# Kernel tuning notes

Measured on AMD Instinct MI355X. Metric: run time of the kernel, lower is better.

The kernel has to match this reference:

```python
import jax, jax.numpy as jnp
import numpy as np

VOCAB = 50257
INPUT_DIM = 1024
CUTOFF_ENDS = [0, 10000, 30000, VOCAB]
PROJ_DIMS = [1024, 512, 256]  # input_dim // factor**i, factor=2.0
N_TOKENS = 8192


def setup_inputs() -> dict:
    key = jax.random.key(0)
    ks = jax.random.split(key, 16)
    inp = {
        "x": jax.random.normal(ks[0], (N_TOKENS, INPUT_DIM), dtype=jnp.float32),
        "target": jax.random.randint(ks[1], (N_TOKENS,), 0, VOCAB, dtype=jnp.int64),
    }
    # Per-cluster projection weights (nn.Linear(input_dim, proj_dim, bias=False) -> [proj_dim, input_dim])
    # and output layers (nn.Linear(proj_dim, cluster_size) -> weight [cluster, proj_dim], bias [cluster]).
    for i in range(3):
        cluster = CUTOFF_ENDS[i + 1] - CUTOFF_ENDS[i]
        pd = PROJ_DIMS[i]
        inp[f"p{i}"] = jax.random.normal(ks[2 + 3 * i], (pd, INPUT_DIM), dtype=jnp.float32) * 0.02
        inp[f"w{i}"] = jax.random.normal(ks[3 + 3 * i], (cluster, pd), dtype=jnp.float32) * 0.02
        inp[f"b{i}"] = jnp.zeros((cluster,), dtype=jnp.float32)
    return inp


def reference(x, target, p0, w0, b0, p1, w1, b1, p2, w2, b2):
    # Faithful to torch AdaptiveSoftmax.forward(input, target):
    # per-cluster: gather tokens whose target falls in [l, r), project, classify,
    # cross-entropy. Clusters partition [0, vocab), so every token hits exactly
    # one cluster; we compute each cluster's pipeline densely over all tokens
    # (jit-friendly, no data-dependent shapes) and select per-token via the mask.
    projs, ws, bs = [p0, p1, p2], [w0, w1, w2], [b0, b1, b2]
    target = target.astype(jnp.int32)
    nll = jnp.zeros((x.shape[0],), dtype=x.dtype)
    for i in range(3):
        l, r = CUTOFF_ENDS[i], CUTOFF_ENDS[i + 1]
        mask = (target >= l) & (target < r)
        hidden = jnp.einsum('nd,pd->np', x, projs[i])          # [N, proj_dim]
        logits = jnp.einsum('np,cp->nc', hidden, ws[i]) + bs[i]  # [N, cluster]
        logp = jax.nn.log_softmax(logits, axis=-1)
        t_i = jnp.clip(target - l, 0, r - l - 1)
        nll_i = -jnp.take_along_axis(logp, t_i[:, None], axis=1)[:, 0]
        nll = jnp.where(mask, nll_i, nll)
    loss = nll.sum()  # == sum of per-cluster reduction='sum' cross-entropies
    return loss, nll
```

## Files before the change

kernel.cpp:

```cpp
#include <hip/hip_runtime.h>
#include <cmath>

#define N_TOK 8192
#define DIM 1024

using bf16x8 = __attribute__((ext_vector_type(8))) short;
using f32x4  = __attribute__((ext_vector_type(4))) float;

__device__ __forceinline__ unsigned f2bf(float f) {
  unsigned u = __float_as_uint(f);
  return (u + 0x7fffu + ((u >> 16) & 1u)) >> 16;
}

__device__ __forceinline__ void gll16(const void* g, void* l) {
  __builtin_amdgcn_global_load_lds(
      (const __attribute__((address_space(1))) void*)g,
      (__attribute__((address_space(3))) void*)l, 16, 0, 0);
}

__global__ __launch_bounds__(1024) void k_setup(const int* __restrict__ tgt,
                                                int* __restrict__ cnt,
                                                int* __restrict__ hoff,
                                                int* __restrict__ perm) {
  __shared__ int base[3];
  int t = threadIdx.x;
  if (t < 3) base[t] = 0;
  __syncthreads();
  for (int i = t; i < N_TOK; i += 1024) {
    int tg = tgt[i];
    int cid = (tg < 10000) ? 0 : (tg < 30000 ? 1 : 2);
    int slot = atomicAdd(&base[cid], 1);
    perm[cid * N_TOK + slot] = i;
  }
  __syncthreads();
  if (t < 3) cnt[t] = base[t];
  if (t == 0) {
    hoff[0] = 0;
    hoff[1] = base[0] * 1024;
    hoff[2] = base[0] * 1024 + base[1] * 512;
  }
}

__global__ __launch_bounds__(256) void k_hc(
    const float* __restrict__ x,
    const float* __restrict__ p0, const float* __restrict__ p1, const float* __restrict__ p2,
    const float* __restrict__ w0, const float* __restrict__ w1, const float* __restrict__ w2,
    const int* __restrict__ perm, const int* __restrict__ cnt, const int* __restrict__ hoffs,
    unsigned short* __restrict__ wb, unsigned short* __restrict__ hb) {
  if (blockIdx.z == 0) {
    const int nw0 = 10240000, nw1 = 10240000, nw2 = 5185792;
    const int total4 = (nw0 + nw1 + nw2) >> 2;
    for (int i = blockIdx.x * 256 + threadIdx.x; i < total4; i += 512 * 256) {
      int e = i << 2;
      const float* src;
      if (e < nw0) src = w0 + e;
      else if (e < nw0 + nw1) src = w1 + (e - nw0);
      else src = w2 + (e - nw0 - nw1);
      float4 v = *(const float4*)src;
      uint2 o;
      o.x = f2bf(v.x) | (f2bf(v.y) << 16);
      o.y = f2bf(v.z) | (f2bf(v.w) << 16);
      *(uint2*)(wb + e) = o;
    }
    return;
  }
  const int cid = blockIdx.z - 1;
  const int pd = (cid == 0) ? 1024 : (cid == 1) ? 512 : 256;
  const int count = cnt[cid];
  if (count == 0) return;
  const int nchd = pd >> 7;
  const int chunk = blockIdx.x % nchd;
  const int tile = blockIdx.x / nchd;
  if (tile * 128 >= count) return;
  const int dim0 = chunk * 128, row0 = tile * 128;
  const float* P = (cid == 0) ? p0 : (cid == 1) ? p1 : p2;
  const size_t hoff = (size_t)hoffs[cid];

  __shared__ char pool[34816];
  __shared__ int ptoks[128];
  short* stg = (short*)pool;
  short* Os = (short*)pool;

  const int t = threadIdx.x, wv = t >> 6, lane = t & 63, m = lane & 15, q = lane >> 4;
  const int wr = wv >> 1, wc = wv & 1;

  if (t < 128) {
    int idx = row0 + t;
    ptoks[t] = perm[cid * N_TOK + min(idx, count - 1)];
  }
  __syncthreads();

  const int s0 = t, s1 = t + 256;
  const int r0 = s0 >> 2, g0 = (s0 & 3) ^ ((r0 >> 1) & 3);
  const int r1 = s1 >> 2, g1 = (s1 & 3) ^ ((r1 >> 1) & 3);
  const uint4* srcA0 = (const uint4*)(x + (size_t)ptoks[r0] * DIM) + g0 * 2;
  const uint4* srcA1 = (const uint4*)(x + (size_t)ptoks[r1] * DIM) + g1 * 2;
  const uint4* srcB0 = (const uint4*)(P + (size_t)(dim0 + r0) * DIM) + g0 * 2;
  const uint4* srcB1 = (const uint4*)(P + (size_t)(dim0 + r1) * DIM) + g1 * 2;

  f32x4 acc[4][4];
  #pragma unroll
  for (int rt = 0; rt < 4; ++rt)
    #pragma unroll
    for (int ct = 0; ct < 4; ++ct) acc[rt][ct] = (f32x4){0.f, 0.f, 0.f, 0.f};

  const int sR = (q ^ ((m >> 1) & 3)) * 8;

  {
    uint4 a0 = srcA0[0], a1 = srcA0[1], a2 = srcA1[0], a3 = srcA1[1];
    uint4 b0 = srcB0[0], b1 = srcB0[1], b2 = srcB1[0], b3 = srcB1[1];
    uint4 o;
    o.x = (a0.x >> 16) | (a0.y & 0xFFFF0000u); o.y = (a0.z >> 16) | (a0.w & 0xFFFF0000u);
    o.z = (a1.x >> 16) | (a1.y & 0xFFFF0000u); o.w = (a1.z >> 16) | (a1.w & 0xFFFF0000u);
    *(uint4*)&stg[s0 * 8] = o;
    o.x = (a2.x >> 16) | (a2.y & 0xFFFF0000u); o.y = (a2.z >> 16) | (a2.w & 0xFFFF0000u);
    o.z = (a3.x >> 16) | (a3.y & 0xFFFF0000u); o.w = (a3.z >> 16) | (a3.w & 0xFFFF0000u);
    *(uint4*)&stg[s1 * 8] = o;
    o.x = (b0.x >> 16) | (b0.y & 0xFFFF0000u); o.y = (b0.z >> 16) | (b0.w & 0xFFFF0000u);
    o.z = (b1.x >> 16) | (b1.y & 0xFFFF0000u); o.w = (b1.z >> 16) | (b1.w & 0xFFFF0000u);
    *(uint4*)&stg[4096 + s0 * 8] = o;
    o.x = (b2.x >> 16) | (b2.y & 0xFFFF0000u); o.y = (b2.z >> 16) | (b2.w & 0xFFFF0000u);
    o.z = (b3.x >> 16) | (b3.y & 0xFFFF0000u); o.w = (b3.z >> 16) | (b3.w & 0xFFFF0000u);
    *(uint4*)&stg[4096 + s1 * 8] = o;
  }

  int p = 0;
  for (int ks = 0; ks < 32; ++ks) {
    __syncthreads();
    const bool nxt = (ks + 1) < 32;
    uint4 a0, a1, a2, a3, b0, b1, b2, b3;
    if (nxt) {
      int ko = (ks + 1) * 8;
      a0 = srcA0[ko]; a1 = srcA0[ko + 1]; a2 = srcA1[ko]; a3 = srcA1[ko + 1];
      b0 = srcB0[ko]; b1 = srcB0[ko + 1]; b2 = srcB1[ko]; b3 = srcB1[ko + 1];
    }
    short* SAp = stg + p * 8192;
    short* SBp = SAp + 4096;
    bf16x8 af[4];
    #pragma unroll
    for (int rt = 0; rt < 4; ++rt)
      af[rt] = *(bf16x8*)&SAp[(wr * 64 + rt * 16 + m) * 32 + sR];
    #pragma unroll
    for (int ct = 0; ct < 4; ++ct) {
      bf16x8 bb = *(bf16x8*)&SBp[(wc * 64 + ct * 16 + m) * 32 + sR];
      #pragma unroll
      for (int rt = 0; rt < 4; ++rt)
        acc[rt][ct] = __builtin_amdgcn_mfma_f32_16x16x32_bf16(af[rt], bb, acc[rt][ct], 0, 0, 0);
    }
    if (nxt) {
      short* DA = stg + (p ^ 1) * 8192;
      short* DB = DA + 4096;
      uint4 o;
      o.x = (a0.x >> 16) | (a0.y & 0xFFFF0000u); o.y = (a0.z >> 16) | (a0.w & 0xFFFF0000u);
      o.z = (a1.x >> 16) | (a1.y & 0xFFFF0000u); o.w = (a1.z >> 16) | (a1.w & 0xFFFF0000u);
      *(uint4*)&DA[s0 * 8] = o;
      o.x = (a2.x >> 16) | (a2.y & 0xFFFF0000u); o.y = (a2.z >> 16) | (a2.w & 0xFFFF0000u);
      o.z = (a3.x >> 16) | (a3.y & 0xFFFF0000u); o.w = (a3.z >> 16) | (a3.w & 0xFFFF0000u);
      *(uint4*)&DA[s1 * 8] = o;
      o.x = (b0.x >> 16) | (b0.y & 0xFFFF0000u); o.y = (b0.z >> 16) | (b0.w & 0xFFFF0000u);
      o.z = (b1.x >> 16) | (b1.y & 0xFFFF0000u); o.w = (b1.z >> 16) | (b1.w & 0xFFFF0000u);
      *(uint4*)&DB[s0 * 8] = o;
      o.x = (b2.x >> 16) | (b2.y & 0xFFFF0000u); o.y = (b2.z >> 16) | (b2.w & 0xFFFF0000u);
      o.z = (b3.x >> 16) | (b3.y & 0xFFFF0000u); o.w = (b3.z >> 16) | (b3.w & 0xFFFF0000u);
      *(uint4*)&DB[s1 * 8] = o;
    }
    p ^= 1;
  }

  __syncthreads();
  #pragma unroll
  for (int rt = 0; rt < 4; ++rt)
    #pragma unroll
    for (int ct = 0; ct < 4; ++ct)
      #pragma unroll
      for (int rr = 0; rr < 4; ++rr)
        Os[(wr * 64 + rt * 16 + q * 4 + rr) * 136 + wc * 64 + ct * 16 + m] =
            (short)f2bf(acc[rt][ct][rr]);
  __syncthreads();
  {
    int orow = t >> 1, oh = t & 1;
    int slot = row0 + orow;
    if (slot < count) {
      unsigned short* dst = hb + hoff + (size_t)slot * pd + dim0 + oh * 64;
      const short* src = &Os[orow * 136 + oh * 64];
      #pragma unroll
      for (int i = 0; i < 8; ++i)
        *(uint4*)(dst + i * 8) = *(const uint4*)(src + i * 8);
    }
  }
}

__global__ __launch_bounds__(256) void k_lse(
    const unsigned short* __restrict__ hb, const unsigned short* __restrict__ wb,
    const float* __restrict__ b0_, const float* __restrict__ b1_, const float* __restrict__ b2_,
    const int* __restrict__ tgt, const int* __restrict__ perm,
    const int* __restrict__ cnt, const int* __restrict__ hoffs,
    float* __restrict__ psum, float* __restrict__ tlog) {
  const int cid = blockIdx.z;
  const int pd     = (cid == 0) ? 1024  : (cid == 1) ? 512   : 256;
  const int cstart = (cid == 0) ? 0     : (cid == 1) ? 10000 : 30000;
  const int csize  = (cid == 0) ? 10000 : (cid == 1) ? 20000 : 20257;
  const size_t woff = (cid == 0) ? 0 : (cid == 1) ? (size_t)10240000 : (size_t)20480000;
  const float* bias = (cid == 0) ? b0_ : (cid == 1) ? b1_ : b2_;
  const int count = cnt[cid];
  if (count == 0) return;
  const unsigned ntile = (unsigned)(count + 127) >> 7;
  const int nchunk = (csize + 127) >> 7;
  const int cpx = (nchunk + 7) >> 3;

  const unsigned d = blockIdx.x;
  const int x8 = d & 7;
  const unsigned g = d >> 3;
  const unsigned ci = g / ntile;
  if (ci >= (unsigned)cpx) return;
  const int chunk = x8 * cpx + (int)ci;
  if (chunk >= nchunk) return;
  const int tile = (int)(g - ci * ntile);
  const int col0 = chunk * 128, row0 = tile * 128;
  const size_t hoff = (size_t)hoffs[cid];

  __shared__ short SA[2][4096];
  __shared__ short SB[2][4096];
  __shared__ int ptoks[128];
  __shared__ int tlocs[128];

  const int t = threadIdx.x, wv = t >> 6, lane = t & 63, m = lane & 15, q = lane >> 4;
  const int wr = wv >> 1, wc = wv & 1;

  if (t < 128) {
    int idx = row0 + t;
    int tok = perm[cid * N_TOK + min(idx, count - 1)];
    ptoks[t] = tok;
    tlocs[t] = tgt[tok] - cstart;
  }

  const int sub = lane >> 2;
  const int gsw = (lane & 3) ^ ((sub >> 1) & 3);
  const unsigned short *pA[2], *pB[2];
  short *lA[2][2], *lB[2][2];
  #pragma unroll
  for (int i = 0; i < 2; ++i) {
    int ia = wv * 2 + i;
    int ra = ia * 16 + sub;
    pA[i] = hb + hoff + (size_t)min(row0 + ra, count - 1) * pd + gsw * 8;
    pB[i] = wb + woff + (size_t)min(col0 + ra, csize - 1) * pd + gsw * 8;
    #pragma unroll
    for (int pp = 0; pp < 2; ++pp) {
      lA[i][pp] = &SA[pp][ia * 512];
      lB[i][pp] = &SB[pp][ia * 512];
    }
  }

  float bc[4];
  #pragma unroll
  for (int ct = 0; ct < 4; ++ct)
    bc[ct] = bias[min(col0 + wc * 64 + ct * 16 + m, csize - 1)];

  f32x4 acc[4][4];
  #pragma unroll
  for (int rt = 0; rt < 4; ++rt)
    #pragma unroll
    for (int ct = 0; ct < 4; ++ct) acc[rt][ct] = (f32x4){0.f, 0.f, 0.f, 0.f};

  const int sR = (q ^ ((m >> 1) & 3)) * 8;
  const int nk = pd >> 5;

  #pragma unroll
  for (int i = 0; i < 2; ++i) { gll16(pA[i], lA[i][0]); gll16(pB[i], lB[i][0]); }

  int p = 0;
  for (int ks = 0; ks < nk; ++ks) {
    __syncthreads();
    if (ks + 1 < nk) {
      int ko = (ks + 1) * 32;
      #pragma unroll
      for (int i = 0; i < 2; ++i) {
        gll16(pA[i] + ko, lA[i][p ^ 1]);
        gll16(pB[i] + ko, lB[i][p ^ 1]);
      }
    }
    bf16x8 af[4];
    #pragma unroll
    for (int rt = 0; rt < 4; ++rt)
      af[rt] = *(bf16x8*)&SA[p][(wr * 64 + rt * 16 + m) * 32 + sR];
    #pragma unroll
    for (int ct = 0; ct < 4; ++ct) {
      bf16x8 bb = *(bf16x8*)&SB[p][(wc * 64 + ct * 16 + m) * 32 + sR];
      #pragma unroll
      for (int rt = 0; rt < 4; ++rt)
        acc[rt][ct] = __builtin_amdgcn_mfma_f32_16x16x32_bf16(af[rt], bb, acc[rt][ct], 0, 0, 0);
    }
    p ^= 1;
  }

  float run[4][4] = {{0.f}}, tcap[4][4] = {{0.f}};
  int tfnd[4][4] = {{0}};
  int tl[4][4];
  #pragma unroll
  for (int rt = 0; rt < 4; ++rt)
    #pragma unroll
    for (int rr = 0; rr < 4; ++rr)
      tl[rt][rr] = tlocs[wr * 64 + rt * 16 + q * 4 + rr];

  #pragma unroll
  for (int ct = 0; ct < 4; ++ct) {
    int colg = col0 + wc * 64 + ct * 16 + m;
    bool cok = colg < csize;
    #pragma unroll
    for (int rt = 0; rt < 4; ++rt)
      #pragma unroll
      for (int rr = 0; rr < 4; ++rr) {
        float val = acc[rt][ct][rr] + bc[ct];
        if (cok) {
          run[rt][rr] += __expf(val);
          if (tl[rt][rr] == colg) { tcap[rt][rr] = val; tfnd[rt][rr] = 1; }
        }
      }
  }

  #pragma unroll
  for (int rt = 0; rt < 4; ++rt)
    #pragma unroll
    for (int rr = 0; rr < 4; ++rr) {
      float v = run[rt][rr];
      v += __shfl_xor(v, 1, 64);
      v += __shfl_xor(v, 2, 64);
      v += __shfl_xor(v, 4, 64);
      v += __shfl_xor(v, 8, 64);
      int rowl = wr * 64 + rt * 16 + q * 4 + rr;
      if (row0 + rowl < count) {
        int tok = ptoks[rowl];
        if (m == 0) atomicAdd(&psum[tok], v);
        if (tfnd[rt][rr]) tlog[tok] = tcap[rt][rr];
      }
    }
}

__global__ __launch_bounds__(1024) void k_final(const float* __restrict__ psum,
                                                const float* __restrict__ tlog,
                                                float* __restrict__ out) {
  __shared__ float part[16];
  int t = threadIdx.x;
  float s = 0.f;
  for (int n = t; n < N_TOK; n += 1024) {
    float v = __logf(psum[n]) - tlog[n];
    out[1 + n] = v;
    s += v;
  }
  #pragma unroll
  for (int off = 32; off > 0; off >>= 1) s += __shfl_down(s, off, 64);
  if ((t & 63) == 0) part[t >> 6] = s;
  __syncthreads();
  if (t < 64) {
    float v = (t < 16) ? part[t] : 0.f;
    #pragma unroll
    for (int off = 8; off > 0; off >>= 1) v += __shfl_down(v, off, 64);
    if (t == 0) out[0] = v;
  }
}

extern "C" void kernel_launch(void* const* d_in, const int* in_sizes, int n_in,
                              void* d_out, int out_size, void* d_ws, size_t ws_size,
                              hipStream_t stream) {
  const float* x  = (const float*)d_in[0];
  const int* tgt  = (const int*)d_in[1];
  const float* p0 = (const float*)d_in[2];
  const float* w0 = (const float*)d_in[3];
  const float* b0 = (const float*)d_in[4];
  const float* p1 = (const float*)d_in[5];
  const float* w1 = (const float*)d_in[6];
  const float* b1 = (const float*)d_in[7];
  const float* p2 = (const float*)d_in[8];
  const float* w2 = (const float*)d_in[9];
  const float* b2 = (const float*)d_in[10];
  float* out = (float*)d_out;

  char* ws = (char*)d_ws;
  int* cnt            = (int*)(ws + 0);
  int* hoff           = (int*)(ws + 64);
  int* perm           = (int*)(ws + 256);
  unsigned short* wb  = (unsigned short*)(ws + 131072);
  unsigned short* hb  = (unsigned short*)(ws + 51462656);
  float* psum         = (float*)(ws + 68239872);
  float* tlog         = (float*)(ws + 68272640);

  hipMemsetAsync(psum, 0, N_TOK * sizeof(float), stream);
  k_setup<<<dim3(1), dim3(1024), 0, stream>>>(tgt, cnt, hoff, perm);
  k_hc<<<dim3(512, 1, 4), dim3(256), 0, stream>>>(x, p0, p1, p2, w0, w1, w2,
                                                  perm, cnt, hoff, wb, hb);
  k_lse<<<dim3(10240, 1, 3), dim3(256), 0, stream>>>(hb, wb, b0, b1, b2, tgt, perm, cnt, hoff,
                                                     psum, tlog);
  k_final<<<dim3(1), dim3(1024), 0, stream>>>(psum, tlog, out);
}
```

Measured before the change: 507.0 us.

## Load GEMM operands directly from global into registers, dropping LDS staging

```diff
diff --git a/kernel.cpp b/kernel.cpp
--- a/kernel.cpp
+++ b/kernel.cpp
@@ -10,12 +10,6 @@
 __device__ __forceinline__ unsigned f2bf(float f) {
   unsigned u = __float_as_uint(f);
   return (u + 0x7fffu + ((u >> 16) & 1u)) >> 16;
-}
-
-__device__ __forceinline__ void gll16(const void* g, void* l) {
-  __builtin_amdgcn_global_load_lds(
-      (const __attribute__((address_space(1))) void*)g,
-      (__attribute__((address_space(3))) void*)l, 16, 0, 0);
 }
 
 __global__ __launch_bounds__(1024) void k_setup(const int* __restrict__ tgt,
@@ -41,7 +35,83 @@
   }
 }
 
-__global__ __launch_bounds__(256) void k_hc(
+template<int PD>
+__device__ __forceinline__ void hid_core(
+    const float* __restrict__ x, const float* __restrict__ P,
+    const int* __restrict__ perm_c, int count, int row0, int dim0,
+    unsigned short* __restrict__ hb_c, int* ptoks, short* Os) {
+  const int t = threadIdx.x, wv = t >> 6, lane = t & 63, m = lane & 15, q = lane >> 4;
+  const int wr = wv >> 1, wc = wv & 1;
+  if (t < 128) {
+    int idx = row0 + t;
+    ptoks[t] = perm_c[min(idx, count - 1)];
+  }
+  __syncthreads();
+
+  const float* aP[4];
+  const float* bP[4];
+  #pragma unroll
+  for (int i = 0; i < 4; ++i) {
+    aP[i] = x + (size_t)ptoks[wr * 64 + i * 16 + m] * DIM + q * 8;
+    bP[i] = P + (size_t)(dim0 + wc * 64 + i * 16 + m) * DIM + q * 8;
+  }
+
+  f32x4 acc[4][4];
+  #pragma unroll
+  for (int rt = 0; rt < 4; ++rt)
+    #pragma unroll
+    for (int ct = 0; ct < 4; ++ct) acc[rt][ct] = (f32x4){0.f, 0.f, 0.f, 0.f};
+
+  #pragma unroll 2
+  for (int k0 = 0; k0 < DIM; k0 += 32) {
+    union { bf16x8 v; unsigned u[4]; } af[4], bf_[4];
+    #pragma unroll
+    for (int i = 0; i < 4; ++i) {
+      uint4 a0 = *(const uint4*)(aP[i] + k0);
+      uint4 a1 = *(const uint4*)(aP[i] + k0 + 4);
+      af[i].u[0] = __builtin_amdgcn_perm(a0.y, a0.x, 0x07060302u);
+      af[i].u[1] = __builtin_amdgcn_perm(a0.w, a0.z, 0x07060302u);
+      af[i].u[2] = __builtin_amdgcn_perm(a1.y, a1.x, 0x07060302u);
+      af[i].u[3] = __builtin_amdgcn_perm(a1.w, a1.z, 0x07060302u);
+      uint4 b0 = *(const uint4*)(bP[i] + k0);
+      uint4 b1 = *(const uint4*)(bP[i] + k0 + 4);
+      bf_[i].u[0] = __builtin_amdgcn_perm(b0.y, b0.x, 0x07060302u);
+      bf_[i].u[1] = __builtin_amdgcn_perm(b0.w, b0.z, 0x07060302u);
+      bf_[i].u[2] = __builtin_amdgcn_perm(b1.y, b1.x, 0x07060302u);
+      bf_[i].u[3] = __builtin_amdgcn_perm(b1.w, b1.z, 0x07060302u);
+    }
+    #pragma unroll
+    for (int ct = 0; ct < 4; ++ct)
+      #pragma unroll
+      for (int rt = 0; rt < 4; ++rt)
+        acc[rt][ct] = __builtin_amdgcn_mfma_f32_16x16x32_bf16(af[rt].v, bf_[ct].v,
+                                                              acc[rt][ct], 0, 0, 0);
+  }
+
+  __syncthreads();
+  #pragma unroll
+  for (int rt = 0; rt < 4; ++rt)
+    #pragma unroll
+    for (int ct = 0; ct < 4; ++ct)
+      #pragma unroll
+      for (int rr = 0; rr < 4; ++rr)
+        Os[(wr * 64 + rt * 16 + q * 4 + rr) * 136 + wc * 64 + ct * 16 + m] =
+            (short)f2bf(acc[rt][ct][rr]);
+  __syncthreads();
+  {
+    int orow = t >> 1, oh = t & 1;
+    int slot = row0 + orow;
+    if (slot < count) {
+      unsigned short* dst = hb_c + (size_t)slot * PD + dim0 + oh * 64;
+      const short* src = &Os[orow * 136 + oh * 64];
+      #pragma unroll
+      for (int i = 0; i < 8; ++i)
+        *(uint4*)(dst + i * 8) = *(const uint4*)(src + i * 8);
+    }
+  }
+}
+
+__global__ __launch_bounds__(256, 3) void k_hc(
     const float* __restrict__ x,
     const float* __restrict__ p0, const float* __restrict__ p1, const float* __restrict__ p2,
     const float* __restrict__ w0, const float* __restrict__ w1, const float* __restrict__ w2,
@@ -74,181 +144,43 @@
   if (tile * 128 >= count) return;
   const int dim0 = chunk * 128, row0 = tile * 128;
   const float* P = (cid == 0) ? p0 : (cid == 1) ? p1 : p2;
-  const size_t hoff = (size_t)hoffs[cid];
-
-  __shared__ char pool[34816];
+  unsigned short* hb_c = hb + hoffs[cid];
+  const int* perm_c = perm + cid * N_TOK;
+
   __shared__ int ptoks[128];
-  short* stg = (short*)pool;
-  short* Os = (short*)pool;
-
+  __shared__ short Os[128 * 136];
+
+  if (cid == 0)      hid_core<1024>(x, P, perm_c, count, row0, dim0, hb_c, ptoks, Os);
+  else if (cid == 1) hid_core<512>(x, P, perm_c, count, row0, dim0, hb_c, ptoks, Os);
+  else               hid_core<256>(x, P, perm_c, count, row0, dim0, hb_c, ptoks, Os);
+}
+
+template<int PD>
+__device__ __forceinline__ void lse_core(
+    const unsigned short* __restrict__ hb_c, const unsigned short* __restrict__ wb_c,
+    const float* __restrict__ bias, const int* __restrict__ tgt,
+    const int* __restrict__ perm_c, int count, int csize, int cstart,
+    int row0, int col0,
+    float* __restrict__ psum, float* __restrict__ tlog,
+    int* ptoks, int* tlocs) {
   const int t = threadIdx.x, wv = t >> 6, lane = t & 63, m = lane & 15, q = lane >> 4;
   const int wr = wv >> 1, wc = wv & 1;
-
   if (t < 128) {
     int idx = row0 + t;
-    ptoks[t] = perm[cid * N_TOK + min(idx, count - 1)];
-  }
-  __syncthreads();
-
-  const int s0 = t, s1 = t + 256;
-  const int r0 = s0 >> 2, g0 = (s0 & 3) ^ ((r0 >> 1) & 3);
-  const int r1 = s1 >> 2, g1 = (s1 & 3) ^ ((r1 >> 1) & 3);
-  const uint4* srcA0 = (const uint4*)(x + (size_t)ptoks[r0] * DIM) + g0 * 2;
-  const uint4* srcA1 = (const uint4*)(x + (size_t)ptoks[r1] * DIM) + g1 * 2;
-  const uint4* srcB0 = (const uint4*)(P + (size_t)(dim0 + r0) * DIM) + g0 * 2;
-  const uint4* srcB1 = (const uint4*)(P + (size_t)(dim0 + r1) * DIM) + g1 * 2;
-
-  f32x4 acc[4][4];
-  #pragma unroll
-  for (int rt = 0; rt < 4; ++rt)
-    #pragma unroll
-    for (int ct = 0; ct < 4; ++ct) acc[rt][ct] = (f32x4){0.f, 0.f, 0.f, 0.f};
-
-  const int sR = (q ^ ((m >> 1) & 3)) * 8;
-
-  {
-    uint4 a0 = srcA0[0], a1 = srcA0[1], a2 = srcA1[0], a3 = srcA1[1];
-    uint4 b0 = srcB0[0], b1 = srcB0[1], b2 = srcB1[0], b3 = srcB1[1];
-    uint4 o;
-    o.x = (a0.x >> 16) | (a0.y & 0xFFFF0000u); o.y = (a0.z >> 16) | (a0.w & 0xFFFF0000u);
-    o.z = (a1.x >> 16) | (a1.y & 0xFFFF0000u); o.w = (a1.z >> 16) | (a1.w & 0xFFFF0000u);
-    *(uint4*)&stg[s0 * 8] = o;
-    o.x = (a2.x >> 16) | (a2.y & 0xFFFF0000u); o.y = (a2.z >> 16) | (a2.w & 0xFFFF0000u);
-    o.z = (a3.x >> 16) | (a3.y & 0xFFFF0000u); o.w = (a3.z >> 16) | (a3.w & 0xFFFF0000u);
-    *(uint4*)&stg[s1 * 8] = o;
-    o.x = (b0.x >> 16) | (b0.y & 0xFFFF0000u); o.y = (b0.z >> 16) | (b0.w & 0xFFFF0000u);
-    o.z = (b1.x >> 16) | (b1.y & 0xFFFF0000u); o.w = (b1.z >> 16) | (b1.w & 0xFFFF0000u);
-    *(uint4*)&stg[4096 + s0 * 8] = o;
-    o.x = (b2.x >> 16) | (b2.y & 0xFFFF0000u); o.y = (b2.z >> 16) | (b2.w & 0xFFFF0000u);
-    o.z = (b3.x >> 16) | (b3.y & 0xFFFF0000u); o.w = (b3.z >> 16) | (b3.w & 0xFFFF0000u);
-    *(uint4*)&stg[4096 + s1 * 8] = o;
-  }
-
-  int p = 0;
-  for (int ks = 0; ks < 32; ++ks) {
-    __syncthreads();
-    const bool nxt = (ks + 1) < 32;
-    uint4 a0, a1, a2, a3, b0, b1, b2, b3;
-    if (nxt) {
-      int ko = (ks + 1) * 8;
-      a0 = srcA0[ko]; a1 = srcA0[ko + 1]; a2 = srcA1[ko]; a3 = srcA1[ko + 1];
-      b0 = srcB0[ko]; b1 = srcB0[ko + 1]; b2 = srcB1[ko]; b3 = srcB1[ko + 1];
-    }
-    short* SAp = stg + p * 8192;
-    short* SBp = SAp + 4096;
-    bf16x8 af[4];
-    #pragma unroll
-    for (int rt = 0; rt < 4; ++rt)
-      af[rt] = *(bf16x8*)&SAp[(wr * 64 + rt * 16 + m) * 32 + sR];
-    #pragma unroll
-    for (int ct = 0; ct < 4; ++ct) {
-      bf16x8 bb = *(bf16x8*)&SBp[(wc * 64 + ct * 16 + m) * 32 + sR];
-      #pragma unroll
-      for (int rt = 0; rt < 4; ++rt)
-        acc[rt][ct] = __builtin_amdgcn_mfma_f32_16x16x32_bf16(af[rt], bb, acc[rt][ct], 0, 0, 0);
-    }
-    if (nxt) {
-      short* DA = stg + (p ^ 1) * 8192;
-      short* DB = DA + 4096;
-      uint4 o;
-      o.x = (a0.x >> 16) | (a0.y & 0xFFFF0000u); o.y = (a0.z >> 16) | (a0.w & 0xFFFF0000u);
-      o.z = (a1.x >> 16) | (a1.y & 0xFFFF0000u); o.w = (a1.z >> 16) | (a1.w & 0xFFFF0000u);
-      *(uint4*)&DA[s0 * 8] = o;
-      o.x = (a2.x >> 16) | (a2.y & 0xFFFF0000u); o.y = (a2.z >> 16) | (a2.w & 0xFFFF0000u);
-      o.z = (a3.x >> 16) | (a3.y & 0xFFFF0000u); o.w = (a3.z >> 16) | (a3.w & 0xFFFF0000u);
-      *(uint4*)&DA[s1 * 8] = o;
-      o.x = (b0.x >> 16) | (b0.y & 0xFFFF0000u); o.y = (b0.z >> 16) | (b0.w & 0xFFFF0000u);
-      o.z = (b1.x >> 16) | (b1.y & 0xFFFF0000u); o.w = (b1.z >> 16) | (b1.w & 0xFFFF0000u);
-      *(uint4*)&DB[s0 * 8] = o;
-      o.x = (b2.x >> 16) | (b2.y & 0xFFFF0000u); o.y = (b2.z >> 16) | (b2.w & 0xFFFF0000u);
-      o.z = (b3.x >> 16) | (b3.y & 0xFFFF0000u); o.w = (b3.z >> 16) | (b3.w & 0xFFFF0000u);
-      *(uint4*)&DB[s1 * 8] = o;
-    }
-    p ^= 1;
-  }
-
-  __syncthreads();
-  #pragma unroll
-  for (int rt = 0; rt < 4; ++rt)
-    #pragma unroll
-    for (int ct = 0; ct < 4; ++ct)
-      #pragma unroll
-      for (int rr = 0; rr < 4; ++rr)
-        Os[(wr * 64 + rt * 16 + q * 4 + rr) * 136 + wc * 64 + ct * 16 + m] =
-            (short)f2bf(acc[rt][ct][rr]);
-  __syncthreads();
-  {
-    int orow = t >> 1, oh = t & 1;
-    int slot = row0 + orow;
-    if (slot < count) {
-      unsigned short* dst = hb + hoff + (size_t)slot * pd + dim0 + oh * 64;
-      const short* src = &Os[orow * 136 + oh * 64];
-      #pragma unroll
-      for (int i = 0; i < 8; ++i)
-        *(uint4*)(dst + i * 8) = *(const uint4*)(src + i * 8);
-    }
-  }
-}
-
-__global__ __launch_bounds__(256) void k_lse(
-    const unsigned short* __restrict__ hb, const unsigned short* __restrict__ wb,
-    const float* __restrict__ b0_, const float* __restrict__ b1_, const float* __restrict__ b2_,
-    const int* __restrict__ tgt, const int* __restrict__ perm,
-    const int* __restrict__ cnt, const int* __restrict__ hoffs,
-    float* __restrict__ psum, float* __restrict__ tlog) {
-  const int cid = blockIdx.z;
-  const int pd     = (cid == 0) ? 1024  : (cid == 1) ? 512   : 256;
-  const int cstart = (cid == 0) ? 0     : (cid == 1) ? 10000 : 30000;
-  const int csize  = (cid == 0) ? 10000 : (cid == 1) ? 20000 : 20257;
-  const size_t woff = (cid == 0) ? 0 : (cid == 1) ? (size_t)10240000 : (size_t)20480000;
-  const float* bias = (cid == 0) ? b0_ : (cid == 1) ? b1_ : b2_;
-  const int count = cnt[cid];
-  if (count == 0) return;
-  const unsigned ntile = (unsigned)(count + 127) >> 7;
-  const int nchunk = (csize + 127) >> 7;
-  const int cpx = (nchunk + 7) >> 3;
-
-  const unsigned d = blockIdx.x;
-  const int x8 = d & 7;
-  const unsigned g = d >> 3;
-  const unsigned ci = g / ntile;
-  if (ci >= (unsigned)cpx) return;
-  const int chunk = x8 * cpx + (int)ci;
-  if (chunk >= nchunk) return;
-  const int tile = (int)(g - ci * ntile);
-  const int col0 = chunk * 128, row0 = tile * 128;
-  const size_t hoff = (size_t)hoffs[cid];
-
-  __shared__ short SA[2][4096];
-  __shared__ short SB[2][4096];
-  __shared__ int ptoks[128];
-  __shared__ int tlocs[128];
-
-  const int t = threadIdx.x, wv = t >> 6, lane = t & 63, m = lane & 15, q = lane >> 4;
-  const int wr = wv >> 1, wc = wv & 1;
-
-  if (t < 128) {
-    int idx = row0 + t;
-    int tok = perm[cid * N_TOK + min(idx, count - 1)];
+    int tok = perm_c[min(idx, count - 1)];
     ptoks[t] = tok;
     tlocs[t] = tgt[tok] - cstart;
   }
-
-  const int sub = lane >> 2;
-  const int gsw = (lane & 3) ^ ((sub >> 1) & 3);
-  const unsigned short *pA[2], *pB[2];
-  short *lA[2][2], *lB[2][2];
-  #pragma unroll
-  for (int i = 0; i < 2; ++i) {
-    int ia = wv * 2 + i;
-    int ra = ia * 16 + sub;
-    pA[i] = hb + hoff + (size_t)min(row0 + ra, count - 1) * pd + gsw * 8;
-    pB[i] = wb + woff + (size_t)min(col0 + ra, csize - 1) * pd + gsw * 8;
-    #pragma unroll
-    for (int pp = 0; pp < 2; ++pp) {
-      lA[i][pp] = &SA[pp][ia * 512];
-      lB[i][pp] = &SB[pp][ia * 512];
-    }
+  __syncthreads();
+
+  const unsigned short* aP[4];
+  const unsigned short* bP[4];
+  #pragma unroll
+  for (int i = 0; i < 4; ++i) {
+    int ra = min(row0 + wr * 64 + i * 16 + m, count - 1);
+    aP[i] = hb_c + (size_t)ra * PD + q * 8;
+    int cb = min(col0 + wc * 64 + i * 16 + m, csize - 1);
+    bP[i] = wb_c + (size_t)cb * PD + q * 8;
   }
 
   float bc[4];
@@ -262,35 +194,20 @@
     #pragma unroll
     for (int ct = 0; ct < 4; ++ct) acc[rt][ct] = (f32x4){0.f, 0.f, 0.f, 0.f};
 
-  const int sR = (q ^ ((m >> 1) & 3)) * 8;
-  const int nk = pd >> 5;
-
-  #pragma unroll
-  for (int i = 0; i < 2; ++i) { gll16(pA[i], lA[i][0]); gll16(pB[i], lB[i][0]); }
-
-  int p = 0;
-  for (int ks = 0; ks < nk; ++ks) {
-    __syncthreads();
-    if (ks + 1 < nk) {
-      int ko = (ks + 1) * 32;
-      #pragma unroll
-      for (int i = 0; i < 2; ++i) {
-        gll16(pA[i] + ko, lA[i][p ^ 1]);
-        gll16(pB[i] + ko, lB[i][p ^ 1]);
-      }
-    }
-    bf16x8 af[4];
-    #pragma unroll
-    for (int rt = 0; rt < 4; ++rt)
-      af[rt] = *(bf16x8*)&SA[p][(wr * 64 + rt * 16 + m) * 32 + sR];
-    #pragma unroll
-    for (int ct = 0; ct < 4; ++ct) {
-      bf16x8 bb = *(bf16x8*)&SB[p][(wc * 64 + ct * 16 + m) * 32 + sR];
+  #pragma unroll 4
+  for (int k0 = 0; k0 < PD; k0 += 32) {
+    bf16x8 af[4], bf_[4];
+    #pragma unroll
+    for (int i = 0; i < 4; ++i) {
+      af[i] = *(const bf16x8*)(aP[i] + k0);
+      bf_[i] = *(const bf16x8*)(bP[i] + k0);
+    }
+    #pragma unroll
+    for (int ct = 0; ct < 4; ++ct)
       #pragma unroll
       for (int rt = 0; rt < 4; ++rt)
-        acc[rt][ct] = __builtin_amdgcn_mfma_f32_16x16x32_bf16(af[rt], bb, acc[rt][ct], 0, 0, 0);
-    }
-    p ^= 1;
+        acc[rt][ct] = __builtin_amdgcn_mfma_f32_16x16x32_bf16(af[rt], bf_[ct],
+                                                              acc[rt][ct], 0, 0, 0);
   }
 
   float run[4][4] = {{0.f}}, tcap[4][4] = {{0.f}};
@@ -334,6 +251,51 @@
         if (tfnd[rt][rr]) tlog[tok] = tcap[rt][rr];
       }
     }
+}
+
+__global__ __launch_bounds__(256, 3) void k_lse(
+    const unsigned short* __restrict__ hb, const unsigned short* __restrict__ wb,
+    const float* __restrict__ b0_, const float* __restrict__ b1_, const float* __restrict__ b2_,
+    const int* __restrict__ tgt, const int* __restrict__ perm,
+    const int* __restrict__ cnt, const int* __restrict__ hoffs,
+    float* __restrict__ psum, float* __restrict__ tlog) {
+  const int cid = blockIdx.z;
+  const int cstart = (cid == 0) ? 0     : (cid == 1) ? 10000 : 30000;
+  const int csize  = (cid == 0) ? 10000 : (cid == 1) ? 20000 : 20257;
+  const size_t woff = (cid == 0) ? 0 : (cid == 1) ? (size_t)10240000 : (size_t)20480000;
+  const float* bias = (cid == 0) ? b0_ : (cid == 1) ? b1_ : b2_;
+  const int count = cnt[cid];
+  if (count == 0) return;
+  const unsigned ntile = (unsigned)(count + 127) >> 7;
+  const int nchunk = (csize + 127) >> 7;
+  const int cpx = (nchunk + 7) >> 3;
+
+  const unsigned d = blockIdx.x;
+  const int x8 = d & 7;
+  const unsigned g = d >> 3;
+  const unsigned ci = g / ntile;
+  if (ci >= (unsigned)cpx) return;
+  const int chunk = x8 * cpx + (int)ci;
+  if (chunk >= nchunk) return;
+  const int tile = (int)(g - ci * ntile);
+  const int col0 = chunk * 128, row0 = tile * 128;
+
+  const unsigned short* hb_c = hb + hoffs[cid];
+  const unsigned short* wb_c = wb + woff;
+  const int* perm_c = perm + cid * N_TOK;
+
+  __shared__ int ptoks[128];
+  __shared__ int tlocs[128];
+
+  if (cid == 0)
+    lse_core<1024>(hb_c, wb_c, bias, tgt, perm_c, count, csize, cstart, row0, col0,
+                   psum, tlog, ptoks, tlocs);
+  else if (cid == 1)
+    lse_core<512>(hb_c, wb_c, bias, tgt, perm_c, count, csize, cstart, row0, col0,
+                  psum, tlog, ptoks, tlocs);
+  else
+    lse_core<256>(hb_c, wb_c, bias, tgt, perm_c, count, csize, cstart, row0, col0,
+                  psum, tlog, ptoks, tlocs);
 }
 
 __global__ __launch_bounds__(1024) void k_final(const float* __restrict__ psum,
```

Result: slower. 772.8 us (+52.4%).
